# Kernel tuning notes

Hardware: AMD Instinct MI355X
Metric: run time of the kernel (lower is better)

Reference implementation:

```python
import jax, jax.numpy as jnp
import numpy as np

U, P, D, B, H = 8192, 4096, 64, 1024, 50
EPS = 1e-8  # torch.cosine_similarity eps


def setup_inputs() -> dict:
    key = jax.random.key(0)
    ks = jax.random.split(key, 11)
    inp = {}
    for i, name in enumerate(["A_up", "A_up_NR", "A_up_FR", "A_up_TR", "A_up_UR"]):
        inp[name] = jax.random.uniform(ks[i], (U, P), jnp.float32)
    inp["user_emb"] = jax.random.normal(ks[5], (U, D), jnp.float32) * 0.1
    inp["post_emb"] = jax.random.normal(ks[6], (P, D), jnp.float32) * 0.1
    inp["user_model"] = jax.random.normal(ks[7], (U, 4), jnp.float32)
    inp["X_source_id"] = jax.random.randint(ks[8], (B,), 0, P)
    inp["X_user_id"] = jax.random.randint(ks[9], (B,), 0, U)
    inp["X_rumer_id"] = jax.random.randint(ks[10], (B, H), 0, U)
    return inp


def _forward(A, user_emb, post_emb, W, X_source_id, X_rumer_id):
    # A: [5,U,P] stacked relations [base, NR, FR, TR, UR].
    # 2-layer LightGCN-style propagation, batched across all 5 relations:
    #   u_k = A @ p_{k-1};  p_k = A^T @ u_{k-1}
    u0, p0 = user_emb, post_emb
    u1 = jnp.einsum('rup,pd->rud', A, p0)    # [5,U,D]
    p1 = jnp.einsum('rup,ud->rpd', A, u0)    # [5,P,D]
    u2 = jnp.einsum('rup,rpd->rud', A, p1)
    p2 = jnp.einsum('rup,rud->rpd', A, u1)
    # fused stack+mean over the 3 layer outputs (x0, x1, x2)
    Xu = (u0[None] + u1 + u2) / 3.0          # [5,U,D]
    X_post_full = (p0 + p1[0] + p2[0]) / 3.0  # [P,D] (base relation only)

    base = Xu[0]   # [U,D]
    rel = Xu[1:]   # [4,U,D]

    # cosine similarity of base users vs each relation variant
    n0 = jnp.linalg.norm(base, axis=1)                # [U]
    nr = jnp.linalg.norm(rel, axis=2)                 # [4,U]
    sim = jnp.sum(base[None] * rel, axis=2) / jnp.maximum(n0[None] * nr, EPS)
    sim = sim.T                                       # [U,4]
    mask = (sim == sim.max(axis=1, keepdims=True)).astype(sim.dtype)
    simm = mask * sim
    var = jnp.log(jnp.std(simm, axis=1, ddof=1) + 1.0)  # [U]; torch.std is unbiased

    user = jnp.transpose(rel, (1, 0, 2))                 # [U,4,D]
    user_embedding = jnp.einsum('ua,uad->ud', W, user)   # [U,D]
    # note: post_embedding = A_pu @ user_embedding is computed in the original
    # get_Userembedding but never used by forward's outputs; omitted.

    X_post = X_post_full[X_source_id]                    # [B,D]
    Xvu = base[X_rumer_id]                               # [B,H,D]
    Xv = var[X_rumer_id]                                 # [B,H]
    X_var_user = jnp.einsum('bh,bhd->bd', Xv, Xvu)       # [B,D]
    AugUser = jnp.mean(user_embedding[X_rumer_id], axis=1)  # [B,D]
    X_mean_user = jnp.mean(Xvu, axis=1)                  # [B,D]
    return X_post, X_var_user, AugUser, X_mean_user


def reference(A_up, A_up_NR, A_up_FR, A_up_TR, A_up_UR,
              user_emb, post_emb, user_model,
              X_source_id, X_user_id, X_rumer_id):
    A = jnp.stack([A_up, A_up_NR, A_up_FR, A_up_TR, A_up_UR], axis=0)
    return _forward(A, user_emb, post_emb, user_model, X_source_id, X_rumer_id)
```

## Files before the change

kernel.cpp:

```cpp
#include <hip/hip_runtime.h>
#include <math.h>

#define U_DIM 8192
#define P_DIM 4096
#define B_DIM 1024
#define H_DIM 50
#define EPSV  1e-8f

typedef __attribute__((ext_vector_type(8))) short short8;
typedef __attribute__((ext_vector_type(4))) float f32x4;

struct APtrs { const float* p[5]; };

__device__ inline unsigned short f2bf(float f) {
    unsigned int u = __float_as_uint(f);
    u += 0x7FFFu + ((u >> 16) & 1u);
    return (unsigned short)(u >> 16);
}

__global__ __launch_bounds__(256) void transpose_bf16_k(
    const float* __restrict__ in, unsigned short* __restrict__ out,
    int K, long strideIn, long strideOut)
{
    __shared__ float t[64][65];
    const int tid = threadIdx.x;
    const int kb  = blockIdx.x * 64;
    const float* ip = in + (size_t)blockIdx.y * strideIn + (size_t)kb * 64;
#pragma unroll
    for (int j = 0; j < 16; ++j) {
        int idx = tid + j * 256;
        t[idx >> 6][idx & 63] = ip[idx];
    }
    __syncthreads();
    unsigned short* op = out + (size_t)blockIdx.y * strideOut;
#pragma unroll
    for (int j = 0; j < 16; ++j) {
        int idx = tid + j * 256;
        int d = idx >> 6, k = idx & 63;
        op[(size_t)d * K + kb + k] = f2bf(t[k][d]);
    }
}

template<bool TRANS>
__global__ __launch_bounds__(256, 4) void gemm_n64(
    APtrs Aps, const unsigned short* __restrict__ BT, float* __restrict__ C,
    long strideBT, long strideC, int kseg)
{
    const int K   = TRANS ? U_DIM : P_DIM;
    const int tid  = threadIdx.x;
    const int wid  = tid >> 6;
    const int lane = tid & 63;
    const int l15  = lane & 15;
    const int kg   = (lane >> 4) << 3;
    const int m0   = blockIdx.x * 128 + wid * 32;
    const float* Ag = Aps.p[blockIdx.y];
    const unsigned short* Bp = BT + (size_t)blockIdx.y * strideBT;
    float* Cp = C + (size_t)blockIdx.y * strideC;
    const long k0 = (long)blockIdx.z * kseg + kg;

    const float* a0;
    if (!TRANS) a0 = Ag + (size_t)(m0 + l15) * K + k0;
    else        a0 = Ag + (size_t)k0 * P_DIM + m0 + l15;
    const unsigned short* b0 = Bp + (size_t)l15 * K + k0;

    const size_t a16 = (size_t)16 * K;
    const size_t K16 = (size_t)16 * K;

    f32x4 acc[2][4] = {};

#define LOADA(A_, kk_) do {                                                     \
    if (!TRANS) {                                                               \
        const float* ap_ = a0 + (kk_);                                          \
        A_[0] = *(const float4*)ap_;          A_[1] = *(const float4*)(ap_ + 4);\
        A_[2] = *(const float4*)(ap_ + a16);  A_[3] = *(const float4*)(ap_ + a16 + 4); \
    } else {                                                                    \
        const float* ap_ = a0 + (size_t)(kk_) * P_DIM;                          \
        A_[0].x = ap_[0 * (size_t)P_DIM];      A_[0].y = ap_[1 * (size_t)P_DIM];\
        A_[0].z = ap_[2 * (size_t)P_DIM];      A_[0].w = ap_[3 * (size_t)P_DIM];\
        A_[1].x = ap_[4 * (size_t)P_DIM];      A_[1].y = ap_[5 * (size_t)P_DIM];\
        A_[1].z = ap_[6 * (size_t)P_DIM];      A_[1].w = ap_[7 * (size_t)P_DIM];\
        A_[2].x = ap_[0 * (size_t)P_DIM + 16]; A_[2].y = ap_[1 * (size_t)P_DIM + 16]; \
        A_[2].z = ap_[2 * (size_t)P_DIM + 16]; A_[2].w = ap_[3 * (size_t)P_DIM + 16]; \
        A_[3].x = ap_[4 * (size_t)P_DIM + 16]; A_[3].y = ap_[5 * (size_t)P_DIM + 16]; \
        A_[3].z = ap_[6 * (size_t)P_DIM + 16]; A_[3].w = ap_[7 * (size_t)P_DIM + 16]; \
    }                                                                           \
} while (0)

#define LOADB(B_, kk_) do {                                                     \
    B_[0] = *(const short8*)(b0 + (kk_));                                       \
    B_[1] = *(const short8*)(b0 + K16 + (kk_));                                 \
    B_[2] = *(const short8*)(b0 + 2 * K16 + (kk_));                             \
    B_[3] = *(const short8*)(b0 + 3 * K16 + (kk_));                             \
} while (0)

#define STEP(A_, B_) do {                                                       \
    short8 a0f, a1f;                                                            \
    a0f[0] = (short)f2bf(A_[0].x); a0f[1] = (short)f2bf(A_[0].y);               \
    a0f[2] = (short)f2bf(A_[0].z); a0f[3] = (short)f2bf(A_[0].w);               \
    a0f[4] = (short)f2bf(A_[1].x); a0f[5] = (short)f2bf(A_[1].y);               \
    a0f[6] = (short)f2bf(A_[1].z); a0f[7] = (short)f2bf(A_[1].w);               \
    a1f[0] = (short)f2bf(A_[2].x); a1f[1] = (short)f2bf(A_[2].y);               \
    a1f[2] = (short)f2bf(A_[2].z); a1f[3] = (short)f2bf(A_[2].w);               \
    a1f[4] = (short)f2bf(A_[3].x); a1f[5] = (short)f2bf(A_[3].y);               \
    a1f[6] = (short)f2bf(A_[3].z); a1f[7] = (short)f2bf(A_[3].w);               \
    _Pragma("unroll")                                                           \
    for (int nt = 0; nt < 4; ++nt) {                                            \
        acc[0][nt] = __builtin_amdgcn_mfma_f32_16x16x32_bf16(a0f, B_[nt], acc[0][nt], 0, 0, 0); \
        acc[1][nt] = __builtin_amdgcn_mfma_f32_16x16x32_bf16(a1f, B_[nt], acc[1][nt], 0, 0, 0); \
    }                                                                           \
} while (0)

    float4 Aa[4], Ab[4];
    short8 Ba[4], Bb[4];
    LOADA(Aa, 0); LOADB(Ba, 0);
    for (int kk = 0; kk < kseg; kk += 64) {
        LOADA(Ab, kk + 32); LOADB(Bb, kk + 32);
        STEP(Aa, Ba);
        if (kk + 64 < kseg) { LOADA(Aa, kk + 64); LOADB(Ba, kk + 64); }
        STEP(Ab, Bb);
    }

#undef LOADA
#undef LOADB
#undef STEP

    const int rb4 = (lane >> 4) << 2;
#pragma unroll
    for (int mt = 0; mt < 2; ++mt)
#pragma unroll
        for (int nt = 0; nt < 4; ++nt)
#pragma unroll
            for (int i = 0; i < 4; ++i) {
                int row = m0 + (mt << 4) + rb4 + i;
                atomicAdd(&Cp[((size_t)row << 6) + (nt << 4) + l15], acc[mt][nt][i]);
            }
}

__device__ inline float wsum(float v) {
#pragma unroll
    for (int off = 32; off > 0; off >>= 1) v += __shfl_xor(v, off, 64);
    return v;
}

__global__ __launch_bounds__(256) void user_stats_k(
    const float* __restrict__ u0, const float* __restrict__ u1,
    const float* __restrict__ u2, const float* __restrict__ W,
    float* __restrict__ base_o, float* __restrict__ var_o, float* __restrict__ ue_o)
{
    int u    = blockIdx.x * 4 + (threadIdx.x >> 6);
    int lane = threadIdx.x & 63;
    size_t ud = ((size_t)u << 6) + lane;

    float b0 = u0[ud];
    float xu[5];
#pragma unroll
    for (int r = 0; r < 5; ++r)
        xu[r] = (b0 + u1[(size_t)r * U_DIM * 64 + ud] + u2[(size_t)r * U_DIM * 64 + ud]) * (1.0f / 3.0f);

    float base = xu[0];
    float n0 = sqrtf(wsum(base * base));
    float sim[4];
#pragma unroll
    for (int a = 0; a < 4; ++a) {
        float d  = wsum(base * xu[a + 1]);
        float nr = sqrtf(wsum(xu[a + 1] * xu[a + 1]));
        sim[a] = d / fmaxf(n0 * nr, EPSV);
    }
    float smax = fmaxf(fmaxf(sim[0], sim[1]), fmaxf(sim[2], sim[3]));
    float ssum = 0.0f;
    float simm[4];
#pragma unroll
    for (int a = 0; a < 4; ++a) { simm[a] = (sim[a] == smax) ? sim[a] : 0.0f; ssum += simm[a]; }
    float mean = ssum * 0.25f;
    float vs = 0.0f;
#pragma unroll
    for (int a = 0; a < 4; ++a) { float t = simm[a] - mean; vs += t * t; }
    vs *= (1.0f / 3.0f);
    float var = logf(sqrtf(vs) + 1.0f);

    float ue = 0.0f;
#pragma unroll
    for (int a = 0; a < 4; ++a) ue += W[((size_t)u << 2) + a] * xu[a + 1];

    base_o[ud] = base;
    ue_o[ud]   = ue;
    if (lane == 0) var_o[u] = var;
}

__global__ __launch_bounds__(256) void gather_k(
    const float* __restrict__ p0, const float* __restrict__ p1r0, const float* __restrict__ p2,
    const float* __restrict__ base, const float* __restrict__ var, const float* __restrict__ ue,
    const int* __restrict__ src_id, const int* __restrict__ rumer, float* __restrict__ out)
{
    int b    = blockIdx.x * 4 + (threadIdx.x >> 6);
    int lane = threadIdx.x & 63;

    int sp = src_id[b];
    size_t spd = ((size_t)sp << 6) + lane;
    out[((size_t)b << 6) + lane] = (p0[spd] + p1r0[spd] + p2[spd]) * (1.0f / 3.0f);

    float xv = 0.0f, xm = 0.0f, au = 0.0f;
    for (int h = 0; h < H_DIM; ++h) {
        int uu = rumer[b * H_DIM + h];
        size_t uud = ((size_t)uu << 6) + lane;
        float bv = base[uud];
        xv += var[uu] * bv;
        xm += bv;
        au += ue[uud];
    }
    out[((size_t)(B_DIM     + b) << 6) + lane] = xv;
    out[((size_t)(2 * B_DIM + b) << 6) + lane] = au * (1.0f / H_DIM);
    out[((size_t)(3 * B_DIM + b) << 6) + lane] = xm * (1.0f / H_DIM);
}

extern "C" void kernel_launch(void* const* d_in, const int* in_sizes, int n_in,
                              void* d_out, int out_size, void* d_ws, size_t ws_size,
                              hipStream_t stream)
{
    const float* u0 = (const float*)d_in[5];
    const float* p0 = (const float*)d_in[6];
    const float* W  = (const float*)d_in[7];
    const int* src   = (const int*)d_in[8];
    const int* rumer = (const int*)d_in[10];
    float* out = (float*)d_out;

    APtrs Ap;
    for (int r = 0; r < 5; ++r) Ap.p[r] = (const float*)d_in[r];

    float* u1   = (float*)d_ws;
    float* p1   = u1 + 5l * U_DIM * 64;
    float* p2   = p1 + 5l * P_DIM * 64;
    float* u2   = p2 + (long)P_DIM * 64;
    float* base = u2 + 5l * U_DIM * 64;
    float* var  = base + (long)U_DIM * 64;
    float* ue   = var + U_DIM;

    unsigned short* p0T = (unsigned short*)base;
    unsigned short* u0T = p0T + 64l * P_DIM;
    unsigned short* p1T = (unsigned short*)base;
    unsigned short* u1T = p1T + 5l * 64 * P_DIM;

    size_t zero_bytes = (size_t)(5l * U_DIM * 64 + 5l * P_DIM * 64 + (long)P_DIM * 64 + 5l * U_DIM * 64) * sizeof(float);
    hipMemsetAsync(d_ws, 0, zero_bytes, stream);

    transpose_bf16_k<<<dim3(P_DIM / 64, 1), 256, 0, stream>>>(p0, p0T, P_DIM, 0, 0);
    transpose_bf16_k<<<dim3(U_DIM / 64, 1), 256, 0, stream>>>(u0, u0T, U_DIM, 0, 0);

    gemm_n64<false><<<dim3(64, 5, 4), 256, 0, stream>>>(Ap, p0T, u1, 0, (long)U_DIM * 64, 1024);
    gemm_n64<true ><<<dim3(32, 5, 8), 256, 0, stream>>>(Ap, u0T, p1, 0, (long)P_DIM * 64, 1024);

    transpose_bf16_k<<<dim3(P_DIM / 64, 5), 256, 0, stream>>>(p1, p1T, P_DIM, (long)P_DIM * 64, 64l * P_DIM);
    transpose_bf16_k<<<dim3(U_DIM / 64, 1), 256, 0, stream>>>(u1, u1T, U_DIM, 0, 0);

    gemm_n64<false><<<dim3(64, 5, 4), 256, 0, stream>>>(Ap, p1T, u2, 64l * P_DIM, (long)U_DIM * 64, 1024);
    gemm_n64<true ><<<dim3(32, 1, 32), 256, 0, stream>>>(Ap, u1T, p2, 0, 0, 256);

    user_stats_k<<<U_DIM / 4, 256, 0, stream>>>(u0, u1, u2, W, base, var, ue);
    gather_k<<<B_DIM / 4, 256, 0, stream>>>(p0, p1, p2, base, var, ue, src, rumer, out);
}
```

Measured before the change: 1.006 ms.

## Pre-convert adjacency matrices to bf16 and a transposed copy for GEMMs

Adds a conversion kernel that reads each fp32 adjacency matrix once and writes a row-major bf16 copy plus, when workspace allows, a transposed bf16 copy. The four propagation GEMMs then stream bf16 instead of fp32, halving A traffic per pass, and the A^T products can use contiguous vector loads instead of strided scalar loads. Split-K depth is also doubled for more parallelism. The cost is an extra full pass over A plus up to 400MB of workspace writes, with a fallback to the old fp32 path if the workspace is too small.

```diff
diff --git a/kernel.cpp b/kernel.cpp
--- a/kernel.cpp
+++ b/kernel.cpp
@@ -8,6 +8,8 @@
 #define EPSV  1e-8f
 
 typedef __attribute__((ext_vector_type(8))) short short8;
+typedef __attribute__((ext_vector_type(4))) short short4v;
+typedef __attribute__((ext_vector_type(2))) short short2v;
 typedef __attribute__((ext_vector_type(4))) float f32x4;
 
 struct APtrs { const float* p[5]; };
@@ -18,6 +20,38 @@
     return (unsigned short)(u >> 16);
 }
 
+__global__ __launch_bounds__(256) void conv_bf16_k(
+    APtrs Aps, unsigned short* __restrict__ rm, unsigned short* __restrict__ tp)
+{
+    __shared__ float t[64][65];
+    const int tid = threadIdx.x;
+    const int p0 = blockIdx.x * 64;
+    const int m0 = blockIdx.y * 64;
+    const size_t rbase = (size_t)blockIdx.z * ((size_t)U_DIM * P_DIM);
+    const float* ip = Aps.p[blockIdx.z];
+    unsigned short* rp = rm + rbase;
+    const int c4 = (tid & 15) * 4;
+#pragma unroll
+    for (int j = 0; j < 4; ++j) {
+        int row = (tid >> 4) + j * 16;
+        float4 v = *(const float4*)(ip + (size_t)(m0 + row) * P_DIM + p0 + c4);
+        short4v w = { (short)f2bf(v.x), (short)f2bf(v.y), (short)f2bf(v.z), (short)f2bf(v.w) };
+        *(short4v*)(rp + (size_t)(m0 + row) * P_DIM + p0 + c4) = w;
+        t[row][c4 + 0] = v.x; t[row][c4 + 1] = v.y;
+        t[row][c4 + 2] = v.z; t[row][c4 + 3] = v.w;
+    }
+    if (!tp) return;
+    __syncthreads();
+    unsigned short* op = tp + rbase;
+#pragma unroll
+    for (int j = 0; j < 4; ++j) {
+        int prow = (tid >> 4) + j * 16;
+        short4v w = { (short)f2bf(t[c4 + 0][prow]), (short)f2bf(t[c4 + 1][prow]),
+                      (short)f2bf(t[c4 + 2][prow]), (short)f2bf(t[c4 + 3][prow]) };
+        *(short4v*)(op + (size_t)(p0 + prow) * U_DIM + m0 + c4) = w;
+    }
+}
+
 __global__ __launch_bounds__(256) void transpose_bf16_k(
     const float* __restrict__ in, unsigned short* __restrict__ out,
     int K, long strideIn, long strideOut)
@@ -42,7 +76,85 @@
 }
 
 template<bool TRANS>
-__global__ __launch_bounds__(256, 4) void gemm_n64(
+__global__ __launch_bounds__(256, 4) void gemm_bf16(
+    const unsigned short* __restrict__ Abase, long strideA,
+    const unsigned short* __restrict__ BT, long strideBT,
+    float* __restrict__ C, long strideC, int K, int kseg)
+{
+    const int tid  = threadIdx.x;
+    const int wid  = tid >> 6;
+    const int lane = tid & 63;
+    const int l15  = lane & 15;
+    const int kg   = (lane >> 4) << 3;
+    const int m0   = blockIdx.x * 128 + wid * 32;
+    const unsigned short* A  = Abase + (size_t)blockIdx.y * strideA;
+    const unsigned short* Bp = BT + (size_t)blockIdx.y * strideBT;
+    float* Cp = C + (size_t)blockIdx.y * strideC;
+    const long k0 = (long)blockIdx.z * kseg + kg;
+
+    const unsigned short* a0;
+    if (!TRANS) a0 = A + (size_t)(m0 + l15) * K + k0;
+    else        a0 = A + (size_t)k0 * P_DIM + m0 + l15;
+    const unsigned short* b0 = Bp + (size_t)l15 * K + k0;
+    const size_t aK16 = (size_t)16 * K;
+
+    f32x4 acc[2][4] = {};
+    short8 Aa[2], Ab[2], Ba[4], Bb[4];
+
+#define LA(R_, kk_) do {                                                        \
+    if (!TRANS) {                                                               \
+        R_[0] = *(const short8*)(a0 + (kk_));                                   \
+        R_[1] = *(const short8*)(a0 + aK16 + (kk_));                            \
+    } else {                                                                    \
+        _Pragma("unroll")                                                       \
+        for (int j = 0; j < 8; ++j) {                                           \
+            R_[0][j] = (short)a0[(size_t)((kk_) + j) * P_DIM];                  \
+            R_[1][j] = (short)a0[(size_t)((kk_) + j) * P_DIM + 16];             \
+        }                                                                       \
+    }                                                                           \
+} while (0)
+
+#define LB(R_, kk_) do {                                                        \
+    R_[0] = *(const short8*)(b0 + (kk_));                                       \
+    R_[1] = *(const short8*)(b0 + aK16 + (kk_));                                \
+    R_[2] = *(const short8*)(b0 + 2 * aK16 + (kk_));                            \
+    R_[3] = *(const short8*)(b0 + 3 * aK16 + (kk_));                            \
+} while (0)
+
+#define STEP(A_, B_) do {                                                       \
+    _Pragma("unroll")                                                           \
+    for (int nt = 0; nt < 4; ++nt) {                                            \
+        acc[0][nt] = __builtin_amdgcn_mfma_f32_16x16x32_bf16(A_[0], B_[nt], acc[0][nt], 0, 0, 0); \
+        acc[1][nt] = __builtin_amdgcn_mfma_f32_16x16x32_bf16(A_[1], B_[nt], acc[1][nt], 0, 0, 0); \
+    }                                                                           \
+} while (0)
+
+    LA(Aa, 0); LB(Ba, 0);
+    for (int kk = 0; kk < kseg; kk += 64) {
+        LA(Ab, kk + 32); LB(Bb, kk + 32);
+        STEP(Aa, Ba);
+        if (kk + 64 < kseg) { LA(Aa, kk + 64); LB(Ba, kk + 64); }
+        STEP(Ab, Bb);
+    }
+
+#undef LA
+#undef LB
+#undef STEP
+
+    const int rb4 = (lane >> 4) << 2;
+#pragma unroll
+    for (int mt = 0; mt < 2; ++mt)
+#pragma unroll
+        for (int nt = 0; nt < 4; ++nt)
+#pragma unroll
+            for (int i = 0; i < 4; ++i) {
+                int row = m0 + (mt << 4) + rb4 + i;
+                atomicAdd(&Cp[((size_t)row << 6) + (nt << 4) + l15], acc[mt][nt][i]);
+            }
+}
+
+template<bool TRANS>
+__global__ __launch_bounds__(256, 4) void gemm_f32(
     APtrs Aps, const unsigned short* __restrict__ BT, float* __restrict__ C,
     long strideBT, long strideC, int kseg)
 {
@@ -62,7 +174,6 @@
     if (!TRANS) a0 = Ag + (size_t)(m0 + l15) * K + k0;
     else        a0 = Ag + (size_t)k0 * P_DIM + m0 + l15;
     const unsigned short* b0 = Bp + (size_t)l15 * K + k0;
-
     const size_t a16 = (size_t)16 * K;
     const size_t K16 = (size_t)16 * K;
 
@@ -93,7 +204,7 @@
     B_[3] = *(const short8*)(b0 + 3 * K16 + (kk_));                             \
 } while (0)
 
-#define STEP(A_, B_) do {                                                       \
+#define STEPF(A_, B_) do {                                                      \
     short8 a0f, a1f;                                                            \
     a0f[0] = (short)f2bf(A_[0].x); a0f[1] = (short)f2bf(A_[0].y);               \
     a0f[2] = (short)f2bf(A_[0].z); a0f[3] = (short)f2bf(A_[0].w);               \
@@ -115,14 +226,14 @@
     LOADA(Aa, 0); LOADB(Ba, 0);
     for (int kk = 0; kk < kseg; kk += 64) {
         LOADA(Ab, kk + 32); LOADB(Bb, kk + 32);
-        STEP(Aa, Ba);
+        STEPF(Aa, Ba);
         if (kk + 64 < kseg) { LOADA(Aa, kk + 64); LOADB(Ba, kk + 64); }
-        STEP(Ab, Bb);
+        STEPF(Ab, Bb);
     }
 
 #undef LOADA
 #undef LOADB
-#undef STEP
+#undef STEPF
 
     const int rb4 = (lane >> 4) << 2;
 #pragma unroll
@@ -240,20 +351,53 @@
     unsigned short* p1T = (unsigned short*)base;
     unsigned short* u1T = p1T + 5l * 64 * P_DIM;
 
-    size_t zero_bytes = (size_t)(5l * U_DIM * 64 + 5l * P_DIM * 64 + (long)P_DIM * 64 + 5l * U_DIM * 64) * sizeof(float);
+    const size_t interm_floats = 7872512;
+    const size_t UP = (size_t)U_DIM * P_DIM;
+    unsigned short* A_rm = (unsigned short*)((float*)d_ws + interm_floats);
+    unsigned short* A_T  = A_rm + 5 * UP;
+    const size_t need_B = interm_floats * 4 + 5 * UP * 2;
+    const size_t need_A = need_B + 5 * UP * 2;
+
+    const size_t zero_bytes = (size_t)(5l * U_DIM * 64 + 5l * P_DIM * 64 +
+                                       (long)P_DIM * 64 + 5l * U_DIM * 64) * sizeof(float);
     hipMemsetAsync(d_ws, 0, zero_bytes, stream);
 
     transpose_bf16_k<<<dim3(P_DIM / 64, 1), 256, 0, stream>>>(p0, p0T, P_DIM, 0, 0);
     transpose_bf16_k<<<dim3(U_DIM / 64, 1), 256, 0, stream>>>(u0, u0T, U_DIM, 0, 0);
 
-    gemm_n64<false><<<dim3(64, 5, 4), 256, 0, stream>>>(Ap, p0T, u1, 0, (long)U_DIM * 64, 1024);
-    gemm_n64<true ><<<dim3(32, 5, 8), 256, 0, stream>>>(Ap, u0T, p1, 0, (long)P_DIM * 64, 1024);
-
-    transpose_bf16_k<<<dim3(P_DIM / 64, 5), 256, 0, stream>>>(p1, p1T, P_DIM, (long)P_DIM * 64, 64l * P_DIM);
-    transpose_bf16_k<<<dim3(U_DIM / 64, 1), 256, 0, stream>>>(u1, u1T, U_DIM, 0, 0);
-
-    gemm_n64<false><<<dim3(64, 5, 4), 256, 0, stream>>>(Ap, p1T, u2, 64l * P_DIM, (long)U_DIM * 64, 1024);
-    gemm_n64<true ><<<dim3(32, 1, 32), 256, 0, stream>>>(Ap, u1T, p2, 0, 0, 256);
+    if (ws_size >= need_B) {
+        const bool tierA = (ws_size >= need_A);
+        conv_bf16_k<<<dim3(P_DIM / 64, U_DIM / 64, 5), 256, 0, stream>>>(
+            Ap, A_rm, tierA ? A_T : (unsigned short*)nullptr);
+
+        gemm_bf16<false><<<dim3(64, 5, 8), 256, 0, stream>>>(
+            A_rm, (long)UP, p0T, 0, u1, (long)U_DIM * 64, P_DIM, 512);
+        if (tierA)
+            gemm_bf16<false><<<dim3(32, 5, 16), 256, 0, stream>>>(
+                A_T, (long)UP, u0T, 0, p1, (long)P_DIM * 64, U_DIM, 512);
+        else
+            gemm_bf16<true><<<dim3(32, 5, 16), 256, 0, stream>>>(
+                A_rm, (long)UP, u0T, 0, p1, (long)P_DIM * 64, U_DIM, 512);
+
+        transpose_bf16_k<<<dim3(P_DIM / 64, 5), 256, 0, stream>>>(p1, p1T, P_DIM, (long)P_DIM * 64, 64l * P_DIM);
+        transpose_bf16_k<<<dim3(U_DIM / 64, 1), 256, 0, stream>>>(u1, u1T, U_DIM, 0, 0);
+
+        gemm_bf16<false><<<dim3(64, 5, 8), 256, 0, stream>>>(
+            A_rm, (long)UP, p1T, 64l * P_DIM, u2, (long)U_DIM * 64, P_DIM, 512);
+        if (tierA)
+            gemm_bf16<false><<<dim3(32, 1, 32), 256, 0, stream>>>(
+                A_T, 0, u1T, 0, p2, 0, U_DIM, 256);
+        else
+            gemm_bf16<true><<<dim3(32, 1, 32), 256, 0, stream>>>(
+                A_rm, 0, u1T, 0, p2, 0, U_DIM, 256);
+    } else {
+        gemm_f32<false><<<dim3(64, 5, 4), 256, 0, stream>>>(Ap, p0T, u1, 0, (long)U_DIM * 64, 1024);
+        gemm_f32<true ><<<dim3(32, 5, 8), 256, 0, stream>>>(Ap, u0T, p1, 0, (long)P_DIM * 64, 1024);
+        transpose_bf16_k<<<dim3(P_DIM / 64, 5), 256, 0, stream>>>(p1, p1T, P_DIM, (long)P_DIM * 64, 64l * P_DIM);
+        transpose_bf16_k<<<dim3(U_DIM / 64, 1), 256, 0, stream>>>(u1, u1T, U_DIM, 0, 0);
+        gemm_f32<false><<<dim3(64, 5, 4), 256, 0, stream>>>(Ap, p1T, u2, 64l * P_DIM, (long)U_DIM * 64, 1024);
+        gemm_f32<true ><<<dim3(32, 1, 32), 256, 0, stream>>>(Ap, u1T, p2, 0, 0, 256);
+    }
 
     user_stats_k<<<U_DIM / 4, 256, 0, stream>>>(u0, u1, u2, W, base, var, ue);
     gather_k<<<B_DIM / 4, 256, 0, stream>>>(p0, p1, p2, base, var, ue, src, rumer, out);
```

Result: slower. 1.133 ms (+12.7%).
